# Kernel optimization log

Hardware: AMD Instinct MI355X
Metric: run time of the kernel (lower is better)

Reference implementation:

```python
import jax, jax.numpy as jnp
import numpy as np

TOP_K = 2  # config.moe_config['moe_top_k']


def setup_inputs() -> dict:
    key = jax.random.key(0)
    k1, k2, k3, k4 = jax.random.split(key, 4)
    B, S, H, F, E = 2, 1024, 1024, 2048, 8
    def init(k, shape, fan_in):
        return jax.random.normal(k, shape, jnp.float32) / np.float32(np.sqrt(fan_in))
    return {
        "hidden_states": jax.random.normal(k1, (B, S, H), jnp.float32),
        "router_w": init(k2, (H, E), H),          # Linear(hidden, E, bias=False)
        "W1": init(k3, (E, H, 2 * F), H),          # per-expert Linear(hidden, 2*ffn)
        "W2": init(k4, (E, F, H), F),              # per-expert Linear(ffn, hidden)
    }


def reference(hidden_states, router_w, W1, W2):
    B, S, H = hidden_states.shape
    E = router_w.shape[1]
    x = hidden_states.reshape(-1, H)                      # [N, H], N = B*S
    N = x.shape[0]

    # router: logits -> fp32 softmax -> top-k -> renormalize (matches torch)
    logits = x @ router_w                                  # [N, E]
    probs = jax.nn.softmax(logits.astype(jnp.float32), axis=-1)
    rw, sel = jax.lax.top_k(probs, TOP_K)                  # [N, k]
    rw = rw / rw.sum(axis=-1, keepdims=True)
    rw = rw.astype(x.dtype)

    # combine weights per (token, expert); top-k experts are distinct so add==set
    cw = jnp.zeros((N, E), x.dtype).at[jnp.arange(N)[:, None], sel].add(rw)

    # per-expert SwiGLU MLP over all tokens, masked combine (full-capacity MoE)
    h = jnp.einsum('nh,ehf->enf', x, W1)                   # [E, N, 2F]
    a, b = jnp.split(h, 2, axis=-1)                        # gate, value halves
    g = jax.nn.silu(a) * b                                 # [E, N, F]
    y = jnp.einsum('enf,efh->enh', g, W2)                  # [E, N, H]
    out = jnp.einsum('enh,ne->nh', y, cw)                  # weighted scatter-combine
    return out.reshape(B, S, H)
```

## Files before the change

kernel.cpp:

```cpp
#include <hip/hip_runtime.h>
#include <hip/hip_bf16.h>

#define H_DIM 1024
#define E_NUM 8
#define F_DIM 2048
#define N_TOK 2048
typedef unsigned int uint;
typedef short bf16x8 __attribute__((ext_vector_type(8)));
typedef float f32x4 __attribute__((ext_vector_type(4)));

#define WS_CNT   0
#define WS_LIST  256
#define WS_W     (WS_LIST + 8*N_TOK*4)
#define WS_G     131072
#define WS_Y     (WS_G + 4096*2048*2)
#define WS_XB    WS_Y


static __device__ __forceinline__ uint f2bf(float f) {
    uint u = __builtin_bit_cast(uint, f);
    return (u + 0x7FFFu + ((u >> 16) & 1u)) >> 16;
}
static __device__ __forceinline__ float bflo(uint u) { return __builtin_bit_cast(float, u << 16); }
static __device__ __forceinline__ float bfhi(uint u) { return __builtin_bit_cast(float, u & 0xFFFF0000u); }
static __device__ __forceinline__ uint cvtpk(float a, float b) {
    uint r;
    asm("v_cvt_pk_bf16_f32 %0, %1, %2" : "=v"(r) : "v"(a), "v"(b));
    return r;
}
static __device__ __forceinline__ void gload_lds16(const void* g, void* l) {
    __builtin_amdgcn_global_load_lds(
        (const __attribute__((address_space(1))) unsigned int*)g,
        (__attribute__((address_space(3))) unsigned int*)l,
        16, 0, 0);
}

__global__ __launch_bounds__(256) void cvt_x_kernel(const float* __restrict__ x,
                                                    unsigned short* __restrict__ xb)
{
    int c = blockIdx.x * 256 + threadIdx.x;
    int row = c >> 7, b = c & 127;
    int t = b >> 3, s = b & 7;
    int klo = t*64 + (s >> 2)*32 + (s & 3)*4;
    const float* xr = x + (size_t)row * H_DIM;
    float4 lo = *(const float4*)(xr + klo);
    float4 hi = *(const float4*)(xr + klo + 16);
    uint4 o;
    o.x = cvtpk(lo.x, lo.y); o.y = cvtpk(lo.z, lo.w);
    o.z = cvtpk(hi.x, hi.y); o.w = cvtpk(hi.z, hi.w);
    *(uint4*)(xb + (size_t)row * H_DIM + b*8) = o;
}

__global__ __launch_bounds__(256) void router_kernel(
    const float* __restrict__ x, const float* __restrict__ rw,
    int* __restrict__ cnt, int* __restrict__ list, float* __restrict__ w_entry)
{
    int wave = threadIdx.x >> 6, lane = threadIdx.x & 63;
    int n = blockIdx.x * 4 + wave;
    const float* xr = x + (size_t)n * H_DIM;
    float acc[8] = {0,0,0,0,0,0,0,0};
    #pragma unroll
    for (int i = 0; i < H_DIM/64; ++i) {
        int h = i*64 + lane;
        float xv = xr[h];
        const float4* rr = (const float4*)(rw + (size_t)h*8);
        float4 r0 = rr[0], r1 = rr[1];
        acc[0] += xv*r0.x; acc[1] += xv*r0.y; acc[2] += xv*r0.z; acc[3] += xv*r0.w;
        acc[4] += xv*r1.x; acc[5] += xv*r1.y; acc[6] += xv*r1.z; acc[7] += xv*r1.w;
    }
    #pragma unroll
    for (int e = 0; e < 8; ++e) {
        float v = acc[e];
        #pragma unroll
        for (int off = 32; off; off >>= 1) v += __shfl_xor(v, off);
        acc[e] = v;
    }
    int e0 = 0;
    #pragma unroll
    for (int e = 1; e < 8; ++e) if (acc[e] > acc[e0]) e0 = e;
    int e1 = -1;
    #pragma unroll
    for (int e = 0; e < 8; ++e) if (e != e0 && (e1 < 0 || acc[e] > acc[e1])) e1 = e;
    float w0 = 1.0f / (1.0f + __expf(acc[e1] - acc[e0]));
    float w1 = 1.0f - w0;
    if (lane == 0) {
        int p0 = atomicAdd(&cnt[e0], 1);
        list[e0*N_TOK + p0] = n*2;
        w_entry[n*2] = w0;
        int p1 = atomicAdd(&cnt[e1], 1);
        list[e1*N_TOK + p1] = n*2 + 1;
        w_entry[n*2+1] = w1;
    }
}

template<int IS_G1>
__global__ __launch_bounds__(256, 2) void moe_gemm_kernel(
    const unsigned short* __restrict__ Asrc, const float* __restrict__ W,
    const int* __restrict__ cnt, const int* __restrict__ list,
    const float* __restrict__ w_entry, unsigned short* __restrict__ dst)
{
    constexpr int KTOT  = IS_G1 ? H_DIM : F_DIM;
    constexpr int BLD   = IS_G1 ? 2*F_DIM : H_DIM;
    constexpr int DLD   = IS_G1 ? F_DIM : H_DIM;
    constexpr int ALD   = IS_G1 ? H_DIM : F_DIM;
    constexpr int NNT   = IS_G1 ? 32 : 16;
    constexpr int NMT   = 16;
    constexpr int BSROW = IS_G1 ? 512 : 256;
    constexpr int NJ    = IS_G1 ? 4 : 2;
    constexpr int NBS   = IS_G1 ? 4 : 2;

    __shared__ __align__(16) unsigned short As[128*64];
    __shared__ __align__(16) uint Bs[32*(IS_G1 ? 128 : 64)];
    __shared__ int   s_entry[128];
    __shared__ float s_wrow[128];

    constexpr int nb = NMT * NNT * E_NUM;
    constexpr int chunk = nb >> 3;
    int bid = blockIdx.x;
    int f  = (bid & 7) * chunk + (bid >> 3);
    int mt = f % NMT;
    int nt = (f / NMT) % NNT;
    int e  = f / (NMT * NNT);

    const int c = cnt[e];
    if (mt * 128 >= c) return;
    const int tid = threadIdx.x;

    if (tid < 128) {
        int r = mt*128 + tid;
        int rr = r < c ? r : c - 1;
        int ent = list[e*N_TOK + rr];
        s_entry[tid] = ent;
        if constexpr (!IS_G1) s_wrow[tid] = w_entry[ent];
    }
    __syncthreads();

    const int lane = tid & 63, wid = tid >> 6;
    const int wr = wid >> 1, wc = wid & 1;
    const int l15 = lane & 15, lg = lane >> 4;

    const unsigned short* a_src[4];
    #pragma unroll
    for (int i = 0; i < 4; ++i) {
        int sl  = wid*4096 + i*1024 + lane*16;
        int row = sl >> 7;
        int kb  = ((sl >> 4) & 7) ^ (row & 7);
        int ent = s_entry[row];
        int arow = IS_G1 ? (ent >> 1) : ent;
        a_src[i] = Asrc + (size_t)arow * ALD + kb*8;
    }

    const float* Wb = W + (size_t)e * (size_t)(IS_G1 ? H_DIM*2*F_DIM : F_DIM*H_DIM);
    const float* b_src[NBS]; int b_dst[NBS];
    #pragma unroll
    for (int s = 0; s < NBS; ++s) {
        int q = tid + s*256;
        int kp, c4, gc;
        if constexpr (IS_G1) {
            kp = q >> 5; c4 = q & 31;
            gc = (c4 < 16) ? (nt*64 + 4*c4) : (F_DIM + nt*64 + 4*(c4-16));
        } else {
            kp = q >> 4; c4 = q & 15;
            gc = nt*64 + 4*c4;
        }
        b_src[s] = Wb + (size_t)(2*kp) * BLD + gc;
        b_dst[s] = (kp*BSROW + c4*16) ^ ((kp & 4) << 4);
    }

    int a_addr[4][2];
    #pragma unroll
    for (int m = 0; m < 4; ++m)
        #pragma unroll
        for (int kk = 0; kk < 2; ++kk) {
            int row = wr*64 + m*16 + l15;
            a_addr[m][kk] = row*128 + ((kk*64 + lg*16) ^ ((row & 7) << 4));
        }
    int b_base[NJ][2];
    const int xorv = ((2*lg) & 4) << 4;
    #pragma unroll
    for (int j = 0; j < NJ; ++j) {
        int cb = IS_G1 ? ((j < 2) ? (wc*2 + j) : (4 + wc*2 + (j-2))) : (wc*2 + j);
        int co = ((cb*16 + l15) * 4) ^ xorv;
        #pragma unroll
        for (int kk = 0; kk < 2; ++kk)
            b_base[j][kk] = (kk*16 + 2*lg)*BSROW + co;
    }

    f32x4 acc[4][NJ];
    #pragma unroll
    for (int m = 0; m < 4; ++m)
        #pragma unroll
        for (int j = 0; j < NJ; ++j) acc[m][j] = (f32x4){0.f,0.f,0.f,0.f};

    for (int k0 = 0; k0 < KTOT; k0 += 64) {
        #pragma unroll
        for (int i = 0; i < 4; ++i)
            gload_lds16(a_src[i] + k0, (char*)As + wid*4096 + i*1024);
        #pragma unroll
        for (int s = 0; s < NBS; ++s) {
            const float* b0 = b_src[s] + (size_t)k0 * BLD;
            float4 r0 = *(const float4*)b0;
            float4 r1 = *(const float4*)(b0 + BLD);
            uint4 w4;
            w4.x = cvtpk(r0.x, r1.x); w4.y = cvtpk(r0.y, r1.y);
            w4.z = cvtpk(r0.z, r1.z); w4.w = cvtpk(r0.w, r1.w);
            *(uint4*)((char*)Bs + b_dst[s]) = w4;
        }
        __syncthreads();

        #pragma unroll
        for (int kk = 0; kk < 2; ++kk) {
            bf16x8 af[4];
            #pragma unroll
            for (int m = 0; m < 4; ++m)
                af[m] = *(const bf16x8*)((const char*)As + a_addr[m][kk]);
            bf16x8 bfr[NJ];
            #pragma unroll
            for (int j = 0; j < NJ; ++j) {
                const char* bb = (const char*)Bs + b_base[j][kk];
                union { uint u[4]; bf16x8 v; } bu;
                bu.u[0] = *(const uint*)(bb);
                bu.u[1] = *(const uint*)(bb + BSROW);
                bu.u[2] = *(const uint*)(bb + 8*BSROW);
                bu.u[3] = *(const uint*)(bb + 9*BSROW);
                bfr[j] = bu.v;
            }
            #pragma unroll
            for (int m = 0; m < 4; ++m)
                #pragma unroll
                for (int j = 0; j < NJ; ++j)
                    acc[m][j] = __builtin_amdgcn_mfma_f32_16x16x32_bf16(af[m], bfr[j], acc[m][j], 0, 0, 0);
        }
        __syncthreads();
    }

    if constexpr (IS_G1) {
        const int pbase = (nt*2 + wc)*32 + (l15 >> 2)*8 + (l15 & 3);
        #pragma unroll
        for (int m = 0; m < 4; ++m)
            #pragma unroll
            for (int jj = 0; jj < 2; ++jj) {
                f32x4 ga = acc[m][jj], gv = acc[m][jj+2];
                #pragma unroll
                for (int i = 0; i < 4; ++i) {
                    int rl = wr*64 + m*16 + lg*4 + i;
                    if (mt*128 + rl < c) {
                        int ent = s_entry[rl];
                        float a = ga[i];
                        float g = (a / (1.f + __expf(-a))) * gv[i];
                        dst[(size_t)ent * DLD + pbase + jj*4] = (unsigned short)f2bf(g);
                    }
                }
            }
    } else {
        #pragma unroll
        for (int m = 0; m < 4; ++m)
            #pragma unroll
            for (int j = 0; j < NJ; ++j) {
                #pragma unroll
                for (int i = 0; i < 4; ++i) {
                    int rl = wr*64 + m*16 + lg*4 + i;
                    if (mt*128 + rl < c) {
                        int ent = s_entry[rl];
                        float v = s_wrow[rl] * acc[m][j][i];
                        int col = nt*64 + wc*32 + j*16 + l15;
                        dst[(size_t)ent * DLD + col] = (unsigned short)f2bf(v);
                    }
                }
            }
    }
}

__global__ __launch_bounds__(256) void combine_kernel(
    const unsigned short* __restrict__ y, float* __restrict__ out)
{
    int gid = blockIdx.x * 256 + threadIdx.x;
    size_t base = (size_t)gid * 8;
    int n = (int)(base >> 10), h = (int)(base & 1023);
    const uint4 a = *(const uint4*)(y + (size_t)(2*n)   * 1024 + h);
    const uint4 b = *(const uint4*)(y + (size_t)(2*n+1) * 1024 + h);
    float4 o0, o1;
    o0.x = bflo(a.x)+bflo(b.x); o0.y = bfhi(a.x)+bfhi(b.x);
    o0.z = bflo(a.y)+bflo(b.y); o0.w = bfhi(a.y)+bfhi(b.y);
    o1.x = bflo(a.z)+bflo(b.z); o1.y = bfhi(a.z)+bfhi(b.z);
    o1.z = bflo(a.w)+bflo(b.w); o1.w = bfhi(a.w)+bfhi(b.w);
    *(float4*)(out + base)     = o0;
    *(float4*)(out + base + 4) = o1;
}

extern "C" void kernel_launch(void* const* d_in, const int* in_sizes, int n_in,
                              void* d_out, int out_size, void* d_ws, size_t ws_size,
                              hipStream_t stream) {
    const float* x  = (const float*)d_in[0];
    const float* rw = (const float*)d_in[1];
    const float* W1 = (const float*)d_in[2];
    const float* W2 = (const float*)d_in[3];
    float* out = (float*)d_out;
    char* ws = (char*)d_ws;
    int*   cnt     = (int*)(ws + WS_CNT);
    int*   list    = (int*)(ws + WS_LIST);
    float* w_entry = (float*)(ws + WS_W);
    unsigned short* g  = (unsigned short*)(ws + WS_G);
    unsigned short* y  = (unsigned short*)(ws + WS_Y);
    unsigned short* xb = (unsigned short*)(ws + WS_XB);

    hipMemsetAsync(cnt, 0, E_NUM * sizeof(int), stream);
    cvt_x_kernel<<<N_TOK*H_DIM/2048, 256, 0, stream>>>(x, xb);
    router_kernel<<<N_TOK/4, 256, 0, stream>>>(x, rw, cnt, list, w_entry);
    moe_gemm_kernel<1><<<16*32*E_NUM, 256, 0, stream>>>(xb, W1, cnt, list, w_entry, g);
    moe_gemm_kernel<0><<<16*16*E_NUM, 256, 0, stream>>>(g,  W2, cnt, list, w_entry, y);
    combine_kernel<<<(out_size/8 + 255)/256, 256, 0, stream>>>(y, out);
}
```

Before: 234.0 us.

## Double-buffer LDS tiles to overlap global loads with MFMA compute in MoE GEMM

```diff
diff --git a/kernel.cpp b/kernel.cpp
--- a/kernel.cpp
+++ b/kernel.cpp
@@ -108,9 +108,12 @@
     constexpr int BSROW = IS_G1 ? 512 : 256;
     constexpr int NJ    = IS_G1 ? 4 : 2;
     constexpr int NBS   = IS_G1 ? 4 : 2;
-
-    __shared__ __align__(16) unsigned short As[128*64];
-    __shared__ __align__(16) uint Bs[32*(IS_G1 ? 128 : 64)];
+    constexpr int NT    = KTOT / 64;
+    constexpr int ABYTES = 128*64*2;
+    constexpr int BBYTES = 32*BSROW;
+
+    __shared__ __align__(16) unsigned short As[2][128*64];
+    __shared__ __align__(16) uint Bs[2][BBYTES/4];
     __shared__ int   s_entry[128];
     __shared__ float s_wrow[128];
 
@@ -192,32 +195,17 @@
         #pragma unroll
         for (int j = 0; j < NJ; ++j) acc[m][j] = (f32x4){0.f,0.f,0.f,0.f};
 
-    for (int k0 = 0; k0 < KTOT; k0 += 64) {
-        #pragma unroll
-        for (int i = 0; i < 4; ++i)
-            gload_lds16(a_src[i] + k0, (char*)As + wid*4096 + i*1024);
-        #pragma unroll
-        for (int s = 0; s < NBS; ++s) {
-            const float* b0 = b_src[s] + (size_t)k0 * BLD;
-            float4 r0 = *(const float4*)b0;
-            float4 r1 = *(const float4*)(b0 + BLD);
-            uint4 w4;
-            w4.x = cvtpk(r0.x, r1.x); w4.y = cvtpk(r0.y, r1.y);
-            w4.z = cvtpk(r0.z, r1.z); w4.w = cvtpk(r0.w, r1.w);
-            *(uint4*)((char*)Bs + b_dst[s]) = w4;
-        }
-        __syncthreads();
-
+    auto compute_step = [&](const char* ab, const char* bb0) {
         #pragma unroll
         for (int kk = 0; kk < 2; ++kk) {
             bf16x8 af[4];
             #pragma unroll
             for (int m = 0; m < 4; ++m)
-                af[m] = *(const bf16x8*)((const char*)As + a_addr[m][kk]);
+                af[m] = *(const bf16x8*)(ab + a_addr[m][kk]);
             bf16x8 bfr[NJ];
             #pragma unroll
             for (int j = 0; j < NJ; ++j) {
-                const char* bb = (const char*)Bs + b_base[j][kk];
+                const char* bb = bb0 + b_base[j][kk];
                 union { uint u[4]; bf16x8 v; } bu;
                 bu.u[0] = *(const uint*)(bb);
                 bu.u[1] = *(const uint*)(bb + BSROW);
@@ -231,8 +219,51 @@
                 for (int j = 0; j < NJ; ++j)
                     acc[m][j] = __builtin_amdgcn_mfma_f32_16x16x32_bf16(af[m], bfr[j], acc[m][j], 0, 0, 0);
         }
+    };
+
+    #pragma unroll
+    for (int i = 0; i < 4; ++i)
+        gload_lds16(a_src[i], (char*)As[0] + wid*4096 + i*1024);
+    {
+        float4 r0[NBS], r1[NBS];
+        #pragma unroll
+        for (int s = 0; s < NBS; ++s) {
+            r0[s] = *(const float4*)(b_src[s]);
+            r1[s] = *(const float4*)(b_src[s] + BLD);
+        }
+        #pragma unroll
+        for (int s = 0; s < NBS; ++s) {
+            uint4 w4;
+            w4.x = cvtpk(r0[s].x, r1[s].x); w4.y = cvtpk(r0[s].y, r1[s].y);
+            w4.z = cvtpk(r0[s].z, r1[s].z); w4.w = cvtpk(r0[s].w, r1[s].w);
+            *(uint4*)((char*)Bs[0] + b_dst[s]) = w4;
+        }
+    }
+    __syncthreads();
+
+    for (int t = 0; t < NT - 1; ++t) {
+        const int cb_ = t & 1, nb_ = cb_ ^ 1;
+        #pragma unroll
+        for (int i = 0; i < 4; ++i)
+            gload_lds16(a_src[i] + (t+1)*64, (char*)As[nb_] + wid*4096 + i*1024);
+        float4 r0[NBS], r1[NBS];
+        #pragma unroll
+        for (int s = 0; s < NBS; ++s) {
+            const float* b0 = b_src[s] + (size_t)(t+1) * 64 * BLD;
+            r0[s] = *(const float4*)b0;
+            r1[s] = *(const float4*)(b0 + BLD);
+        }
+        compute_step((const char*)As[cb_], (const char*)Bs[cb_]);
+        #pragma unroll
+        for (int s = 0; s < NBS; ++s) {
+            uint4 w4;
+            w4.x = cvtpk(r0[s].x, r1[s].x); w4.y = cvtpk(r0[s].y, r1[s].y);
+            w4.z = cvtpk(r0[s].z, r1[s].z); w4.w = cvtpk(r0[s].w, r1[s].w);
+            *(uint4*)((char*)Bs[nb_] + b_dst[s]) = w4;
+        }
         __syncthreads();
     }
+    compute_step((const char*)As[(NT-1) & 1], (const char*)Bs[(NT-1) & 1]);
 
     if constexpr (IS_G1) {
         const int pbase = (nt*2 + wc)*32 + (l15 >> 2)*8 + (l15 & 3);
```

New measurement: 276.1 us. 1.18x slower.
